# Optimization experiments

Hardware: AMD Instinct MI355X
Metric: run time of the kernel (lower is better)

## Reference

```python
import jax, jax.numpy as jnp
import numpy as np

B, S, D, H, F = 8, 1024, 1024, 16, 4096
DH = D // H
EPS = 1e-8
NEG_INF = -1e30


def setup_inputs() -> dict:
    key = jax.random.key(0)
    ks = jax.random.split(key, 12)
    x = jax.random.normal(ks[0], (B, S, D), jnp.float32)
    # variable valid lengths in [S//2, S]; True = keep (valid token)
    lengths = jax.random.randint(ks[1], (B,), S // 2, S + 1)
    src_key_padding_mask = jnp.arange(S)[None, :] < lengths[:, None]
    rel_pos_bias = 0.02 * jax.random.normal(ks[2], (1, H, S, S), jnp.float32)
    w = lambda k, sh, std: std * jax.random.normal(k, sh, jnp.float32)
    std = D ** -0.5
    return {
        'x': x,
        'src_key_padding_mask': src_key_padding_mask,
        'rel_pos_bias': rel_pos_bias,
        'Wq': w(ks[3], (D, D), std),
        'Wk': w(ks[4], (D, D), std),
        'Wv': w(ks[5], (D, D), std),
        'Wo': w(ks[6], (D, D), std),
        'g1': jnp.ones((D,), jnp.float32),
        'g2': jnp.ones((D,), jnp.float32),
        'W1': w(ks[7], (D, F), std),
        'b1': jnp.zeros((F,), jnp.float32),
        'W2': w(ks[8], (F, F and D), F ** -0.5),
        'b2': jnp.zeros((D,), jnp.float32),
    }


def rmsnorm(x, g):
    # x / sqrt(mean(x^2) + eps) * g   (no mean subtraction)
    ms = jnp.mean(x * x, axis=-1, keepdims=True)
    return x * jax.lax.rsqrt(ms + EPS) * g


def attention(h, kpm, rel_pos_bias, Wq, Wk, Wv, Wo):
    b, s, d = h.shape
    q = (h @ Wq).reshape(b, s, H, DH)
    k = (h @ Wk).reshape(b, s, H, DH)
    v = (h @ Wv).reshape(b, s, H, DH)
    scores = jnp.einsum('bqhd,bkhd->bhqk', q, k) / np.sqrt(DH)
    scores = scores + rel_pos_bias
    scores = jnp.where(kpm[:, None, None, :], scores, NEG_INF)
    attn = jax.nn.softmax(scores, axis=-1)
    out = jnp.einsum('bhqk,bkhd->bqhd', attn, v).reshape(b, s, d)
    return out @ Wo


def reference(x, src_key_padding_mask, rel_pos_bias,
              Wq, Wk, Wv, Wo, g1, g2, W1, b1, W2, b2):
    h = rmsnorm(x, g1)
    x = x + attention(h, src_key_padding_mask, rel_pos_bias, Wq, Wk, Wv, Wo)
    h = rmsnorm(x, g2)
    ff = jax.nn.relu(h @ W1 + b1) @ W2 + b2
    return x + ff
```

## Files before the change

### kernel.cpp

```cpp
#include <hip/hip_runtime.h>
#include <stdint.h>

typedef __bf16 bf16;
typedef __bf16 bf16x4 __attribute__((ext_vector_type(4)));
typedef __bf16 bf16x8 __attribute__((ext_vector_type(8)));
typedef float f32x4 __attribute__((ext_vector_type(4)));

constexpr int Bz = 8, S = 1024, D = 1024, NH = 16, DH = 64, F = 4096;

__device__ __forceinline__ bool is_f32(const uint16_t* dt) { return dt[0] == 0; }

__device__ __forceinline__ void ld4(const void* p, size_t idx, bool f32, float o[4]) {
  if (f32) {
    float4 v = *(const float4*)((const float*)p + idx);
    o[0] = v.x; o[1] = v.y; o[2] = v.z; o[3] = v.w;
  } else {
    bf16x4 v = *(const bf16x4*)((const bf16*)p + idx);
    o[0] = v[0]; o[1] = v[1]; o[2] = v[2]; o[3] = v[3];
  }
}

__device__ __forceinline__ float ld1(const void* p, size_t idx, bool f32) {
  return f32 ? ((const float*)p)[idx] : (float)((const bf16*)p)[idx];
}

__device__ __forceinline__ void gload_lds16(const bf16* g, bf16* l) {
  __builtin_amdgcn_global_load_lds(
      (const __attribute__((address_space(1))) void*)g,
      (__attribute__((address_space(3))) void*)l, 16, 0, 0);
}

__global__ void lengths_kernel(const unsigned char* __restrict__ mask,
                               int* __restrict__ lengths) {
  int b = blockIdx.x;
  int esz = (mask[1] == 1) ? 1 : ((mask[1] != 0) ? 2 : 4);
  int cnt = 0;
  for (int s = threadIdx.x; s < S; s += blockDim.x) {
    const unsigned char* p = mask + ((size_t)b * S + s) * esz;
    unsigned v = 0;
    for (int j = 0; j < esz; j++) v |= p[j];
    cnt += (v != 0) ? 1 : 0;
  }
#pragma unroll
  for (int m = 32; m >= 1; m >>= 1) cnt += __shfl_xor(cnt, m);
  __shared__ int sred[4];
  if ((threadIdx.x & 63) == 0) sred[threadIdx.x >> 6] = cnt;
  __syncthreads();
  if (threadIdx.x == 0) lengths[b] = sred[0] + sred[1] + sred[2] + sred[3];
}

__global__ void prep_all(const void* __restrict__ sq, const void* __restrict__ sk,
                         const void* __restrict__ sv, const void* __restrict__ so,
                         const void* __restrict__ s1, const void* __restrict__ s2,
                         bf16* __restrict__ dq, bf16* __restrict__ dk,
                         bf16* __restrict__ dv, bf16* __restrict__ do_,
                         bf16* __restrict__ d1, bf16* __restrict__ d2,
                         const void* __restrict__ rpb, bf16* __restrict__ biasb,
                         const uint16_t* __restrict__ dt) {
  bool f32 = is_f32(dt);
  int t = blockIdx.x;
  int tx = threadIdx.x, ty = threadIdx.y;
  if (t >= 3072) {
    size_t i = ((size_t)(t - 3072) * 256 + ty * 16 + tx) * 4;
    float v[4];
    ld4(rpb, i, f32, v);
    bf16x4 o;
#pragma unroll
    for (int j = 0; j < 4; j++) o[j] = (bf16)(v[j] * 1.4426950408889634f);
    *(bf16x4*)(biasb + i) = o;
    return;
  }
  const void* src;
  bf16* dst;
  int R, C, gx, base;
  if (t < 1024) {
    int wsel = t >> 8;
    base = wsel << 8;
    src = wsel == 0 ? sq : wsel == 1 ? sk : wsel == 2 ? sv : so;
    dst = wsel == 0 ? dq : wsel == 1 ? dk : wsel == 2 ? dv : do_;
    R = 1024; C = 1024; gx = 16;
  } else if (t < 2048) {
    base = 1024; src = s1; dst = d1; R = 1024; C = 4096; gx = 64;
  } else {
    base = 2048; src = s2; dst = d2; R = 4096; C = 1024; gx = 16;
  }
  int rel = t - base;
  int c0 = (rel % gx) * 64, r0 = (rel / gx) * 64;
  __shared__ bf16 tile[64][65];
#pragma unroll
  for (int i = 0; i < 4; i++) {
    int r = ty * 4 + i;
    float v[4];
    ld4(src, (size_t)(r0 + r) * C + c0 + tx * 4, f32, v);
#pragma unroll
    for (int j = 0; j < 4; j++) tile[r][tx * 4 + j] = (bf16)v[j];
  }
  __syncthreads();
#pragma unroll
  for (int i = 0; i < 4; i++) {
    int rr = ty * 4 + i;
    bf16x4 ov;
#pragma unroll
    for (int j = 0; j < 4; j++) ov[j] = tile[tx * 4 + j][rr];
    *(bf16x4*)(dst + (size_t)(c0 + rr) * R + r0 + tx * 4) = ov;
  }
}

template <bool ADD>
__global__ void rmsnorm_kernel(const void* __restrict__ xv, const bf16* __restrict__ add,
                               const void* __restrict__ gv, bf16* __restrict__ y,
                               const uint16_t* __restrict__ dt) {
  bool f32 = is_f32(dt);
  int row = blockIdx.x, t = threadIdx.x;
  float xf[4];
  ld4(xv, (size_t)row * D + t * 4, f32, xf);
  if (ADD) {
    bf16x4 a = *(const bf16x4*)(add + (size_t)row * D + t * 4);
#pragma unroll
    for (int j = 0; j < 4; j++) xf[j] += (float)a[j];
  }
  float ss = xf[0] * xf[0] + xf[1] * xf[1] + xf[2] * xf[2] + xf[3] * xf[3];
#pragma unroll
  for (int m = 32; m >= 1; m >>= 1) ss += __shfl_xor(ss, m);
  __shared__ float sred[4];
  if ((t & 63) == 0) sred[t >> 6] = ss;
  __syncthreads();
  float tot = sred[0] + sred[1] + sred[2] + sred[3];
  float scale = rsqrtf(tot * (1.0f / D) + 1e-8f);
  float gf[4];
  ld4(gv, (size_t)t * 4, f32, gf);
  bf16x4 ov;
#pragma unroll
  for (int j = 0; j < 4; j++) ov[j] = (bf16)(xf[j] * scale * gf[j]);
  *(bf16x4*)(y + (size_t)row * D + t * 4) = ov;
}

template <bool BIAS, bool RELU, bool RES1, bool RES2, bool OUTEXT, bool VT>
__global__ void gemm_nt(const bf16* __restrict__ A, const bf16* __restrict__ Bt,
                        void* __restrict__ Cv, const void* __restrict__ biasv,
                        const void* __restrict__ res1, const bf16* __restrict__ res2,
                        int M, int N, int K, const uint16_t* __restrict__ dt) {
  bool f32 = is_f32(dt);
  __shared__ bf16 As[2 * 4096];
  __shared__ bf16 Bs[2 * 4096];
  const int tid = threadIdx.x, lane = tid & 63, w = tid >> 6;
  const int wm = w >> 1, wn = w & 1;
  const int lid = blockIdx.x;
  const int bm = ((lid & 7) << 3) + ((lid >> 3) & 7);
  const int bn = lid >> 6;
  const int quad = lane >> 4, c = lane & 15;

  f32x4 acc[4][4];
#pragma unroll
  for (int i = 0; i < 4; i++)
#pragma unroll
    for (int j = 0; j < 4; j++)
#pragma unroll
      for (int r = 0; r < 4; r++) acc[i][j][r] = 0.f;

  const bf16* gA = A + (size_t)(bm * 128 + w * 16 + (lane >> 2)) * K + (lane & 3) * 8;
  const bf16* gB = Bt + (size_t)(bn * 128 + w * 16 + (lane >> 2)) * K + (lane & 3) * 8;
  bf16* lA = As + w * 512;
  bf16* lB = Bs + w * 512;
  const size_t rstep = (size_t)64 * K;

  int aoff[4], boff[4];
#pragma unroll
  for (int i = 0; i < 4; i++) {
    aoff[i] = (wm * 64 + i * 16 + c) * 32 + quad * 8;
    boff[i] = (wn * 64 + i * 16 + c) * 32 + quad * 8;
  }

  for (int k0 = 0; k0 < K; k0 += 64) {
    __syncthreads();
#pragma unroll
    for (int p = 0; p < 2; p++) {
      gload_lds16(gA + p * 32, lA + p * 4096);
      gload_lds16(gA + p * 32 + rstep, lA + p * 4096 + 2048);
      gload_lds16(gB + p * 32, lB + p * 4096);
      gload_lds16(gB + p * 32 + rstep, lB + p * 4096 + 2048);
    }
    gA += 64;
    gB += 64;
    __syncthreads();
#pragma unroll
    for (int p = 0; p < 2; p++) {
      bf16x8 af[4], bfr[4];
#pragma unroll
      for (int i = 0; i < 4; i++) af[i] = *(const bf16x8*)(As + p * 4096 + aoff[i]);
#pragma unroll
      for (int i = 0; i < 4; i++) bfr[i] = *(const bf16x8*)(Bs + p * 4096 + boff[i]);
#pragma unroll
      for (int i = 0; i < 4; i++)
#pragma unroll
        for (int j = 0; j < 4; j++)
          acc[i][j] = __builtin_amdgcn_mfma_f32_16x16x32_bf16(af[i], bfr[j], acc[i][j], 0, 0, 0);
    }
  }

  const int m0 = bm * 128 + wm * 64, n0 = bn * 128 + wn * 64;
#pragma unroll
  for (int i = 0; i < 4; i++) {
#pragma unroll
    for (int j = 0; j < 4; j++) {
      int col = n0 + j * 16 + c;
      if (VT) {
        int row0 = m0 + i * 16 + quad * 4;
        int bb = row0 >> 10, s0 = row0 & 1023;
        int hh = col >> 6, dd = col & 63;
        bf16x4 ov;
#pragma unroll
        for (int r = 0; r < 4; r++) ov[r] = (bf16)acc[i][j][r];
        *(bf16x4*)((bf16*)Cv + ((size_t)((bb << 4) + hh) * 64 + dd) * 1024 + s0) = ov;
      } else {
        float bv = BIAS ? ld1(biasv, col, f32) : 0.f;
#pragma unroll
        for (int r = 0; r < 4; r++) {
          int row = m0 + i * 16 + quad * 4 + r;
          size_t idx = (size_t)row * N + col;
          float vv = acc[i][j][r] + bv;
          if (RELU) vv = fmaxf(vv, 0.f);
          if (RES1) vv += ld1(res1, idx, f32);
          if (RES2) vv += (float)res2[idx];
          if (OUTEXT && f32) ((float*)Cv)[idx] = vv;
          else ((bf16*)Cv)[idx] = (bf16)vv;
        }
      }
    }
  }
}

#define SYNC()                            \
  do {                                    \
    __builtin_amdgcn_sched_barrier(0);    \
    __builtin_amdgcn_s_barrier();         \
    __builtin_amdgcn_sched_barrier(0);    \
  } while (0)
#define VMW(n)                                              \
  do {                                                      \
    asm volatile("s_waitcnt vmcnt(" #n ")" ::: "memory");   \
    __builtin_amdgcn_sched_barrier(0);                      \
  } while (0)

#define STA_(nb, rowbase, kb)                                                  \
  do {                                                                         \
    gload_lds16(Ag + (size_t)(rowbase) * K + (kb), &Abuf[nb][(rowbase) * 64]); \
    gload_lds16(Ag + (size_t)((rowbase) + 8) * K + (kb),                       \
                &Abuf[nb][((rowbase) + 8) * 64]);                              \
  } while (0)
#define STB_(nb, rowbase, kb)                                                  \
  do {                                                                         \
    gload_lds16(Bg + (size_t)(rowbase) * K + (kb), &Bbuf[nb][(rowbase) * 64]); \
    gload_lds16(Bg + (size_t)((rowbase) + 8) * K + (kb),                       \
                &Bbuf[nb][((rowbase) + 8) * 64]);                              \
  } while (0)
#define RDA_(MQ, fr, bufsel)                                                          \
  do {                                                                                \
    _Pragma("unroll") for (int ii = 0; ii < 4; ii++) {                                \
      int arow = wm * 128 + ((MQ)*4 + ii) * 16 + c;                                   \
      fr[ii][0] = *(const bf16x8*)&Abuf[bufsel][arow * 64 + ((quad ^ sx) * 8)];       \
      fr[ii][1] = *(const bf16x8*)&Abuf[bufsel][arow * 64 + (((4 + quad) ^ sx) * 8)]; \
    }                                                                                 \
  } while (0)
#define RDB_(NQ, fr, bufsel)                                                          \
  do {                                                                                \
    _Pragma("unroll") for (int jj = 0; jj < 2; jj++) {                                \
      int brow = wn * 64 + ((NQ)*2 + jj) * 16 + c;                                    \
      fr[jj][0] = *(const bf16x8*)&Bbuf[bufsel][brow * 64 + ((quad ^ sx) * 8)];       \
      fr[jj][1] = *(const bf16x8*)&Bbuf[bufsel][brow * 64 + (((4 + quad) ^ sx) * 8)]; \
    }                                                                                 \
  } while (0)

template <int MQ, int NQ>
__device__ __forceinline__ void mm_phase(f32x4 (&acc)[8][4], const bf16x8 (&afr)[4][2],
                                         const bf16x8 (&bfr)[2][2]) {
#pragma unroll
  for (int ii = 0; ii < 4; ii++)
#pragma unroll
    for (int jj = 0; jj < 2; jj++) {
      acc[MQ * 4 + ii][NQ * 2 + jj] = __builtin_amdgcn_mfma_f32_16x16x32_bf16(
          afr[ii][0], bfr[jj][0], acc[MQ * 4 + ii][NQ * 2 + jj], 0, 0, 0);
      acc[MQ * 4 + ii][NQ * 2 + jj] = __builtin_amdgcn_mfma_f32_16x16x32_bf16(
          afr[ii][1], bfr[jj][1], acc[MQ * 4 + ii][NQ * 2 + jj], 0, 0, 0);
    }
}

template <bool BIAS, bool RELU, bool QKV>
__global__ void __launch_bounds__(512, 2) gemm256(
    const bf16* __restrict__ A, const bf16* __restrict__ Bt, bf16* __restrict__ C,
    bf16* __restrict__ C2, const void* __restrict__ biasv, int N, int K,
    const uint16_t* __restrict__ dt) {
  bool f32 = is_f32(dt);
  __shared__ bf16 Abuf[2][256 * 64];
  __shared__ bf16 Bbuf[2][256 * 64];
  const int tid = threadIdx.x, lane = tid & 63, w = tid >> 6;
  const int wm = w >> 2, wn = w & 3;
  const int quad = lane >> 4, c = lane & 15;
  const int sx = c & 7;
  const int nbn = N >> 8;
  const int nwg = gridDim.x;
  const int sid = (blockIdx.x & 7) * (nwg >> 3) + (blockIdx.x >> 3);
  const int bm = sid / nbn, bn = sid % nbn;

  const int lrow = lane >> 3;
  const int lslot = ((lane & 7) ^ lrow) * 8;
  const bf16* Ag = A + (size_t)(bm * 256 + lrow) * K + lslot;
  const bf16* Bg = Bt + (size_t)(bn * 256 + lrow) * K + lslot;

  const int ra0 = wm * 128 + wn * 16;
  const int ra1 = ra0 + 64;
  const int rb0 = (wn >> 1) * 128 + (wn & 1) * 64 + wm * 16;
  const int rb1 = rb0 + 32;

  f32x4 acc[8][4];
#pragma unroll
  for (int i = 0; i < 8; i++)
#pragma unroll
    for (int j = 0; j < 4; j++)
#pragma unroll
      for (int r = 0; r < 4; r++) acc[i][j][r] = 0.f;

  const int nt = K >> 6;

  STA_(0, ra0, 0);
  STA_(0, ra1, 0);
  STB_(0, rb0, 0);
  STB_(0, rb1, 0);
  STA_(1, ra0, 64);
  VMW(2);
  SYNC();

  for (int t = 0; t < nt; ++t) {
    const int buf = t & 1, nb = buf ^ 1;
    const int kb1 = (t + 1) << 6, kb2 = (t + 2) << 6;
    const bool st1 = (t + 1 < nt), st2 = (t + 2 < nt);
    bf16x8 afr[4][2], bfr0[2][2], bfr1[2][2];
    RDA_(0, afr, buf);
    RDB_(0, bfr0, buf);
    if (st1) STA_(nb, ra1, kb1);
    SYNC();
    __builtin_amdgcn_s_setprio(1);
    mm_phase<0, 0>(acc, afr, bfr0);
    __builtin_amdgcn_s_setprio(0);
    VMW(2);
    SYNC();
    RDB_(1, bfr1, buf);
    if (st1) STB_(nb, rb0, kb1);
    SYNC();
    __builtin_amdgcn_s_setprio(1);
    mm_phase<0, 1>(acc, afr, bfr1);
    __builtin_amdgcn_s_setprio(0);
    SYNC();
    RDA_(1, afr, buf);
    if (st2) STA_(buf, ra0, kb2);
    SYNC();
    __builtin_amdgcn_s_setprio(1);
    mm_phase<1, 0>(acc, afr, bfr0);
    __builtin_amdgcn_s_setprio(0);
    SYNC();
    if (st1) STB_(nb, rb1, kb1);
    SYNC();
    __builtin_amdgcn_s_setprio(1);
    mm_phase<1, 1>(acc, afr, bfr1);
    __builtin_amdgcn_s_setprio(0);
    VMW(4);
    SYNC();
  }

  const int m0 = bm * 256 + wm * 128, n0 = bn * 256 + wn * 64;
  if (QKV && n0 >= 2048) {
#pragma unroll
    for (int fi = 0; fi < 8; fi++)
#pragma unroll
      for (int fj = 0; fj < 4; fj++) {
        int vcol = n0 + fj * 16 + c - 2048;
        int hh = vcol >> 6, dd = vcol & 63;
        int row0 = m0 + fi * 16 + quad * 4;
        int bb = row0 >> 10, s0 = row0 & 1023;
        bf16x4 ov;
#pragma unroll
        for (int r = 0; r < 4; r++) ov[r] = (bf16)acc[fi][fj][r];
        *(bf16x4*)(C2 + ((size_t)((bb << 4) + hh) * 64 + dd) * 1024 + s0) = ov;
      }
    return;
  }
  const int ldc = QKV ? 2048 : N;
#pragma unroll
  for (int fi = 0; fi < 8; fi++)
#pragma unroll
    for (int fj = 0; fj < 4; fj++) {
      int col = n0 + fj * 16 + c;
      float bv = BIAS ? ld1(biasv, col, f32) : 0.f;
#pragma unroll
      for (int r = 0; r < 4; r++) {
        int row = m0 + fi * 16 + quad * 4 + r;
        float vv = acc[fi][fj][r] + bv;
        if (RELU) vv = fmaxf(vv, 0.f);
        C[(size_t)row * ldc + col] = (bf16)vv;
      }
    }
}

__global__ void __launch_bounds__(256) attn_kernel(
    const bf16* __restrict__ qk, const bf16* __restrict__ vt,
    const bf16* __restrict__ bias, const int* __restrict__ lengths,
    bf16* __restrict__ out) {
  __shared__ bf16 QPs[64 * 72];
  __shared__ bf16 Ks[64][72];
  __shared__ bf16 Vs[64][72];
  const int tid = threadIdx.x, lane = tid & 63, w = tid >> 6;
  const int id = blockIdx.x;
  const int qt = id >> 7, b = (id >> 4) & 7, h = id & 15;
  const int len = lengths[b];
  const int quad = lane >> 4, c = lane & 15;
  const int r4 = tid >> 2, c4 = tid & 3;

  {
    size_t qrow = (size_t)(b * S + qt * 64 + r4) * 2048 + h * 64 + c4 * 8;
    *(bf16x8*)&QPs[r4 * 72 + c4 * 8] = *(const bf16x8*)&qk[qrow];
    *(bf16x8*)&QPs[r4 * 72 + 32 + c4 * 8] = *(const bf16x8*)&qk[qrow + 32];
  }
  __syncthreads();
  const bf16x8 a0 = *(const bf16x8*)&QPs[(w * 16 + c) * 72 + quad * 8];
  const bf16x8 a1 = *(const bf16x8*)&QPs[(w * 16 + c) * 72 + 32 + quad * 8];

  bf16* Pw = QPs + w * 16 * 72;
  const int xsw = (quad & 2) << 3;
  const int xsr = (c & 8) << 1;

  float l_[4] = {0.f, 0.f, 0.f, 0.f};
  f32x4 o[4];
#pragma unroll
  for (int ni = 0; ni < 4; ni++)
#pragma unroll
    for (int r = 0; r < 4; r++) o[ni][r] = 0.f;

  const bf16* bbp = bias + (size_t)h * S * S + (size_t)(qt * 64 + w * 16 + quad * 4) * S;
  const int nkt = (len + 63) >> 6;

  const size_t KSTEP = (size_t)64 * 2048;
  const bf16* gk = qk + (size_t)(b * S + r4) * 2048 + 1024 + h * 64 + c4 * 8;
  const bf16* gv = vt + ((size_t)((b * 16 + h) * 64 + r4)) * 1024 + c4 * 8;
  bf16x8 kr0 = *(const bf16x8*)gk;
  bf16x8 kr1 = *(const bf16x8*)(gk + 32);
  bf16x8 vr0 = *(const bf16x8*)gv;
  bf16x8 vr1 = *(const bf16x8*)(gv + 32);
  gk += KSTEP;
  gv += 64;

  for (int kt = 0; kt < nkt; kt++) {
    __syncthreads();
    *(bf16x8*)&Ks[r4][c4 * 8] = kr0;
    *(bf16x8*)&Ks[r4][32 + c4 * 8] = kr1;
    *(bf16x8*)&Vs[r4][c4 * 8] = vr0;
    *(bf16x8*)&Vs[r4][32 + c4 * 8] = vr1;
    __syncthreads();

    bf16 br[4][4];
#pragma unroll
    for (int ni = 0; ni < 4; ni++)
#pragma unroll
      for (int r = 0; r < 4; r++) br[ni][r] = bbp[(size_t)r * S + ni * 16 + c];

    if (kt + 1 < nkt) {
      kr0 = *(const bf16x8*)gk;
      kr1 = *(const bf16x8*)(gk + 32);
      vr0 = *(const bf16x8*)gv;
      vr1 = *(const bf16x8*)(gv + 32);
      gk += KSTEP;
      gv += 64;
    }

    f32x4 s[4];
#pragma unroll
    for (int ni = 0; ni < 4; ni++)
#pragma unroll
      for (int r = 0; r < 4; r++) s[ni][r] = 0.f;
#pragma unroll
    for (int ni = 0; ni < 4; ni++) {
      bf16x8 b0 = *(const bf16x8*)&Ks[ni * 16 + c][quad * 8];
      bf16x8 b1 = *(const bf16x8*)&Ks[ni * 16 + c][32 + quad * 8];
      s[ni] = __builtin_amdgcn_mfma_f32_16x16x32_bf16(a0, b0, s[ni], 0, 0, 0);
      s[ni] = __builtin_amdgcn_mfma_f32_16x16x32_bf16(a1, b1, s[ni], 0, 0, 0);
    }

    const bool full = (kt * 64 + 64 <= len);
#pragma unroll
    for (int ni = 0; ni < 4; ni++) {
      int col = kt * 64 + ni * 16 + c;
      bool valid = full || (col < len);
#pragma unroll
      for (int r = 0; r < 4; r++) {
        float p = valid ? exp2f(fmaf(s[ni][r], 0.18033688011112042f, (float)br[ni][r])) : 0.f;
        s[ni][r] = p;
        l_[r] += p;
      }
    }

#pragma unroll
    for (int ni = 0; ni < 4; ni++)
#pragma unroll
      for (int r = 0; r < 4; r++)
        Pw[(quad * 4 + r) * 72 + ((ni * 16 + c) ^ xsw)] = (bf16)s[ni][r];

    bf16x8 p0 = *(const bf16x8*)&Pw[c * 72 + ((quad * 8) ^ xsr)];
    bf16x8 p1 = *(const bf16x8*)&Pw[c * 72 + ((32 + quad * 8) ^ xsr)];
#pragma unroll
    for (int ni = 0; ni < 4; ni++) {
      bf16x8 vb0 = *(const bf16x8*)&Vs[ni * 16 + c][quad * 8];
      bf16x8 vb1 = *(const bf16x8*)&Vs[ni * 16 + c][32 + quad * 8];
      o[ni] = __builtin_amdgcn_mfma_f32_16x16x32_bf16(p0, vb0, o[ni], 0, 0, 0);
      o[ni] = __builtin_amdgcn_mfma_f32_16x16x32_bf16(p1, vb1, o[ni], 0, 0, 0);
    }
    bbp += 64;
  }

  float inv[4];
#pragma unroll
  for (int r = 0; r < 4; r++) {
    float l = l_[r];
    l += __shfl_xor(l, 1);
    l += __shfl_xor(l, 2);
    l += __shfl_xor(l, 4);
    l += __shfl_xor(l, 8);
    inv[r] = 1.f / l;
  }
#pragma unroll
  for (int ni = 0; ni < 4; ni++)
#pragma unroll
    for (int r = 0; r < 4; r++) {
      size_t idx = ((size_t)(b * S + qt * 64 + w * 16 + quad * 4 + r)) * D + h * 64 + ni * 16 + c;
      out[idx] = (bf16)(o[ni][r] * inv[r]);
    }
}

extern "C" void kernel_launch(void* const* d_in, const int* in_sizes, int n_in,
                              void* d_out, int out_size, void* d_ws, size_t ws_size,
                              hipStream_t stream) {
  const void* x = d_in[0];
  const unsigned char* mask = (const unsigned char*)d_in[1];
  const void* rpb = d_in[2];
  const void* Wq = d_in[3];
  const void* Wk = d_in[4];
  const void* Wv = d_in[5];
  const void* Wo = d_in[6];
  const void* g1 = d_in[7];
  const void* g2 = d_in[8];
  const void* W1 = d_in[9];
  const void* b1 = d_in[10];
  const void* W2 = d_in[11];
  const void* b2 = d_in[12];
  const uint16_t* dt = (const uint16_t*)d_in[7];

  char* ws = (char*)d_ws;
  const size_t MB = 1024 * 1024;
  bf16* WqkT = (bf16*)(ws + 0 * MB);
  bf16* WkT = (bf16*)(ws + 2 * MB);
  bf16* WvT = (bf16*)(ws + 4 * MB);
  bf16* WoT = (bf16*)(ws + 6 * MB);
  bf16* W1T = (bf16*)(ws + 8 * MB);
  bf16* W2T = (bf16*)(ws + 16 * MB);
  bf16* hbuf = (bf16*)(ws + 24 * MB);
  bf16* qkbuf = (bf16*)(ws + 40 * MB);
  bf16* d1buf = (bf16*)(ws + 40 * MB);
  bf16* vtbuf = (bf16*)(ws + 72 * MB);
  bf16* biasb = (bf16*)(ws + 88 * MB);
  bf16* a1b = (bf16*)(ws + 56 * MB);
  int* lens = (int*)d_out;

  lengths_kernel<<<dim3(8), dim3(256), 0, stream>>>(mask, lens);
  prep_all<<<dim3(3072 + 16384), dim3(16, 16), 0, stream>>>(
      Wq, Wk, Wv, Wo, W1, W2, WqkT, WkT, WvT, WoT, W1T, W2T, rpb, biasb, dt);

  rmsnorm_kernel<false><<<dim3(8192), dim3(256), 0, stream>>>(x, nullptr, g1, hbuf, dt);
  gemm256<false, false, true><<<dim3(384), dim3(512), 0, stream>>>(
      hbuf, WqkT, qkbuf, vtbuf, nullptr, 3072, 1024, dt);
  attn_kernel<<<dim3(2048), dim3(256), 0, stream>>>(qkbuf, vtbuf, biasb, lens, hbuf);
  gemm_nt<false, false, false, false, false, false><<<dim3(8 * 64), dim3(256), 0, stream>>>(
      hbuf, WoT, d1buf, nullptr, nullptr, nullptr, 8192, 1024, 1024, dt);
  rmsnorm_kernel<true><<<dim3(8192), dim3(256), 0, stream>>>(x, d1buf, g2, hbuf, dt);
  gemm256<true, true, false><<<dim3(512), dim3(512), 0, stream>>>(
      hbuf, W1T, a1b, nullptr, b1, 4096, 1024, dt);
  gemm_nt<true, false, true, true, true, false><<<dim3(8 * 64), dim3(256), 0, stream>>>(
      a1b, W2T, d_out, b2, x, d1buf, 8192, 1024, 4096, dt);

  (void)in_sizes; (void)n_in; (void)out_size; (void)ws_size;
}
```

Before: 536.9 us.

## Read fp32 relative-position bias directly in attention and fold lengths into prep

Removes the separate pass that converted the relative position bias to scaled bf16, and has the attention kernel read the original bias tensor and scale by log2(e) inline. The bias for the next key tile is register-prefetched during the PV MFMAs. The mask-length computation becomes extra blocks of the weight-prep kernel, dropping one launch. This saves a 64MB read plus 32MB write of bias, but attention now reads fp32 bias (twice the bytes per block, scalar loads) and uses more registers.

```diff
diff --git a/kernel.cpp b/kernel.cpp
--- a/kernel.cpp
+++ b/kernel.cpp
@@ -30,44 +30,36 @@
       (__attribute__((address_space(3))) void*)l, 16, 0, 0);
 }
 
-__global__ void lengths_kernel(const unsigned char* __restrict__ mask,
-                               int* __restrict__ lengths) {
-  int b = blockIdx.x;
-  int esz = (mask[1] == 1) ? 1 : ((mask[1] != 0) ? 2 : 4);
-  int cnt = 0;
-  for (int s = threadIdx.x; s < S; s += blockDim.x) {
-    const unsigned char* p = mask + ((size_t)b * S + s) * esz;
-    unsigned v = 0;
-    for (int j = 0; j < esz; j++) v |= p[j];
-    cnt += (v != 0) ? 1 : 0;
-  }
-#pragma unroll
-  for (int m = 32; m >= 1; m >>= 1) cnt += __shfl_xor(cnt, m);
-  __shared__ int sred[4];
-  if ((threadIdx.x & 63) == 0) sred[threadIdx.x >> 6] = cnt;
-  __syncthreads();
-  if (threadIdx.x == 0) lengths[b] = sred[0] + sred[1] + sred[2] + sred[3];
-}
-
 __global__ void prep_all(const void* __restrict__ sq, const void* __restrict__ sk,
                          const void* __restrict__ sv, const void* __restrict__ so,
                          const void* __restrict__ s1, const void* __restrict__ s2,
                          bf16* __restrict__ dq, bf16* __restrict__ dk,
                          bf16* __restrict__ dv, bf16* __restrict__ do_,
                          bf16* __restrict__ d1, bf16* __restrict__ d2,
-                         const void* __restrict__ rpb, bf16* __restrict__ biasb,
+                         const unsigned char* __restrict__ mask,
+                         int* __restrict__ lengths,
                          const uint16_t* __restrict__ dt) {
+  __shared__ bf16 tile[64][65];
+  __shared__ int sred[4];
   bool f32 = is_f32(dt);
   int t = blockIdx.x;
   int tx = threadIdx.x, ty = threadIdx.y;
   if (t >= 3072) {
-    size_t i = ((size_t)(t - 3072) * 256 + ty * 16 + tx) * 4;
-    float v[4];
-    ld4(rpb, i, f32, v);
-    bf16x4 o;
-#pragma unroll
-    for (int j = 0; j < 4; j++) o[j] = (bf16)(v[j] * 1.4426950408889634f);
-    *(bf16x4*)(biasb + i) = o;
+    int b = t - 3072;
+    int tid = ty * 16 + tx;
+    int esz = (mask[1] == 1) ? 1 : ((mask[1] != 0) ? 2 : 4);
+    int cnt = 0;
+    for (int s = tid; s < S; s += 256) {
+      const unsigned char* p = mask + ((size_t)b * S + s) * esz;
+      unsigned v = 0;
+      for (int j = 0; j < esz; j++) v |= p[j];
+      cnt += (v != 0) ? 1 : 0;
+    }
+#pragma unroll
+    for (int m = 32; m >= 1; m >>= 1) cnt += __shfl_xor(cnt, m);
+    if ((tid & 63) == 0) sred[tid >> 6] = cnt;
+    __syncthreads();
+    if (tid == 0) lengths[b] = sred[0] + sred[1] + sred[2] + sred[3];
     return;
   }
   const void* src;
@@ -86,7 +78,6 @@
   }
   int rel = t - base;
   int c0 = (rel % gx) * 64, r0 = (rel / gx) * 64;
-  __shared__ bf16 tile[64][65];
 #pragma unroll
   for (int i = 0; i < 4; i++) {
     int r = ty * 4 + i;
@@ -403,11 +394,12 @@
 
 __global__ void __launch_bounds__(256) attn_kernel(
     const bf16* __restrict__ qk, const bf16* __restrict__ vt,
-    const bf16* __restrict__ bias, const int* __restrict__ lengths,
-    bf16* __restrict__ out) {
+    const void* __restrict__ bias, const int* __restrict__ lengths,
+    bf16* __restrict__ out, const uint16_t* __restrict__ dt) {
   __shared__ bf16 QPs[64 * 72];
   __shared__ bf16 Ks[64][72];
   __shared__ bf16 Vs[64][72];
+  const bool f32 = is_f32(dt);
   const int tid = threadIdx.x, lane = tid & 63, w = tid >> 6;
   const int id = blockIdx.x;
   const int qt = id >> 7, b = (id >> 4) & 7, h = id & 15;
@@ -435,8 +427,9 @@
 #pragma unroll
     for (int r = 0; r < 4; r++) o[ni][r] = 0.f;
 
-  const bf16* bbp = bias + (size_t)h * S * S + (size_t)(qt * 64 + w * 16 + quad * 4) * S;
+  const size_t bb0 = (size_t)h * S * S + (size_t)(qt * 64 + w * 16 + quad * 4) * S + c;
   const int nkt = (len + 63) >> 6;
+  const float LOG2E = 1.4426950408889634f;
 
   const size_t KSTEP = (size_t)64 * 2048;
   const bf16* gk = qk + (size_t)(b * S + r4) * 2048 + 1024 + h * 64 + c4 * 8;
@@ -447,6 +440,12 @@
   bf16x8 vr1 = *(const bf16x8*)(gv + 32);
   gk += KSTEP;
   gv += 64;
+  float brf[4][4];
+#pragma unroll
+  for (int ni = 0; ni < 4; ni++)
+#pragma unroll
+    for (int r = 0; r < 4; r++)
+      brf[ni][r] = ld1(bias, bb0 + (size_t)r * S + ni * 16, f32) * LOG2E;
 
   for (int kt = 0; kt < nkt; kt++) {
     __syncthreads();
@@ -456,12 +455,6 @@
     *(bf16x8*)&Vs[r4][32 + c4 * 8] = vr1;
     __syncthreads();
 
-    bf16 br[4][4];
-#pragma unroll
-    for (int ni = 0; ni < 4; ni++)
-#pragma unroll
-      for (int r = 0; r < 4; r++) br[ni][r] = bbp[(size_t)r * S + ni * 16 + c];
-
     if (kt + 1 < nkt) {
       kr0 = *(const bf16x8*)gk;
       kr1 = *(const bf16x8*)(gk + 32);
@@ -491,7 +484,7 @@
       bool valid = full || (col < len);
 #pragma unroll
       for (int r = 0; r < 4; r++) {
-        float p = valid ? exp2f(fmaf(s[ni][r], 0.18033688011112042f, (float)br[ni][r])) : 0.f;
+        float p = valid ? exp2f(fmaf(s[ni][r], 0.18033688011112042f, brf[ni][r])) : 0.f;
         s[ni][r] = p;
         l_[r] += p;
       }
@@ -505,6 +498,17 @@
 
     bf16x8 p0 = *(const bf16x8*)&Pw[c * 72 + ((quad * 8) ^ xsr)];
     bf16x8 p1 = *(const bf16x8*)&Pw[c * 72 + ((32 + quad * 8) ^ xsr)];
+
+    float brn[4][4];
+    if (kt + 1 < nkt) {
+      const size_t bnext = bb0 + (size_t)(kt + 1) * 64;
+#pragma unroll
+      for (int ni = 0; ni < 4; ni++)
+#pragma unroll
+        for (int r = 0; r < 4; r++)
+          brn[ni][r] = ld1(bias, bnext + (size_t)r * S + ni * 16, f32) * LOG2E;
+    }
+
 #pragma unroll
     for (int ni = 0; ni < 4; ni++) {
       bf16x8 vb0 = *(const bf16x8*)&Vs[ni * 16 + c][quad * 8];
@@ -512,7 +516,12 @@
       o[ni] = __builtin_amdgcn_mfma_f32_16x16x32_bf16(p0, vb0, o[ni], 0, 0, 0);
       o[ni] = __builtin_amdgcn_mfma_f32_16x16x32_bf16(p1, vb1, o[ni], 0, 0, 0);
     }
-    bbp += 64;
+    if (kt + 1 < nkt) {
+#pragma unroll
+      for (int ni = 0; ni < 4; ni++)
+#pragma unroll
+        for (int r = 0; r < 4; r++) brf[ni][r] = brn[ni][r];
+    }
   }
 
   float inv[4];
@@ -564,18 +573,16 @@
   bf16* qkbuf = (bf16*)(ws + 40 * MB);
   bf16* d1buf = (bf16*)(ws + 40 * MB);
   bf16* vtbuf = (bf16*)(ws + 72 * MB);
-  bf16* biasb = (bf16*)(ws + 88 * MB);
   bf16* a1b = (bf16*)(ws + 56 * MB);
   int* lens = (int*)d_out;
 
-  lengths_kernel<<<dim3(8), dim3(256), 0, stream>>>(mask, lens);
-  prep_all<<<dim3(3072 + 16384), dim3(16, 16), 0, stream>>>(
-      Wq, Wk, Wv, Wo, W1, W2, WqkT, WkT, WvT, WoT, W1T, W2T, rpb, biasb, dt);
+  prep_all<<<dim3(3080), dim3(16, 16), 0, stream>>>(
+      Wq, Wk, Wv, Wo, W1, W2, WqkT, WkT, WvT, WoT, W1T, W2T, mask, lens, dt);
 
   rmsnorm_kernel<false><<<dim3(8192), dim3(256), 0, stream>>>(x, nullptr, g1, hbuf, dt);
   gemm256<false, false, true><<<dim3(384), dim3(512), 0, stream>>>(
       hbuf, WqkT, qkbuf, vtbuf, nullptr, 3072, 1024, dt);
-  attn_kernel<<<dim3(2048), dim3(256), 0, stream>>>(qkbuf, vtbuf, biasb, lens, hbuf);
+  attn_kernel<<<dim3(2048), dim3(256), 0, stream>>>(qkbuf, vtbuf, rpb, lens, hbuf, dt);
   gemm_nt<false, false, false, false, false, false><<<dim3(8 * 64), dim3(256), 0, stream>>>(
       hbuf, WoT, d1buf, nullptr, nullptr, nullptr, 8192, 1024, 1024, dt);
   rmsnorm_kernel<true><<<dim3(8192), dim3(256), 0, stream>>>(x, d1buf, g2, hbuf, dt);
```

Measured after the change: 541.8 us. No clear change (+0.9%).

## Double-buffer K/V tiles in attention, add MFMA priority, fold lengths into prep

Applied to the files above, without the earlier changes.

The attention kernel now keeps two LDS buffers for K and V, so the next tile is written to LDS while the current one is being used. This replaces two barriers per iteration with one. The MFMA sections are wrapped in s_setprio to favour matrix-issuing waves. The separate lengths kernel is merged into prep_all as eight extra blocks, which removes one launch. The cost is more LDS per block, which may reduce occupancy.

```diff
diff --git a/kernel.cpp b/kernel.cpp
--- a/kernel.cpp
+++ b/kernel.cpp
@@ -30,44 +30,47 @@
       (__attribute__((address_space(3))) void*)l, 16, 0, 0);
 }
 
-__global__ void lengths_kernel(const unsigned char* __restrict__ mask,
-                               int* __restrict__ lengths) {
-  int b = blockIdx.x;
-  int esz = (mask[1] == 1) ? 1 : ((mask[1] != 0) ? 2 : 4);
-  int cnt = 0;
-  for (int s = threadIdx.x; s < S; s += blockDim.x) {
-    const unsigned char* p = mask + ((size_t)b * S + s) * esz;
-    unsigned v = 0;
-    for (int j = 0; j < esz; j++) v |= p[j];
-    cnt += (v != 0) ? 1 : 0;
-  }
-#pragma unroll
-  for (int m = 32; m >= 1; m >>= 1) cnt += __shfl_xor(cnt, m);
-  __shared__ int sred[4];
-  if ((threadIdx.x & 63) == 0) sred[threadIdx.x >> 6] = cnt;
-  __syncthreads();
-  if (threadIdx.x == 0) lengths[b] = sred[0] + sred[1] + sred[2] + sred[3];
-}
-
 __global__ void prep_all(const void* __restrict__ sq, const void* __restrict__ sk,
                          const void* __restrict__ sv, const void* __restrict__ so,
                          const void* __restrict__ s1, const void* __restrict__ s2,
                          bf16* __restrict__ dq, bf16* __restrict__ dk,
                          bf16* __restrict__ dv, bf16* __restrict__ do_,
                          bf16* __restrict__ d1, bf16* __restrict__ d2,
+                         const unsigned char* __restrict__ mask,
+                         int* __restrict__ lengths,
                          const void* __restrict__ rpb, bf16* __restrict__ biasb,
                          const uint16_t* __restrict__ dt) {
+  __shared__ bf16 tile[64][65];
+  __shared__ int sred[4];
   bool f32 = is_f32(dt);
   int t = blockIdx.x;
   int tx = threadIdx.x, ty = threadIdx.y;
-  if (t >= 3072) {
-    size_t i = ((size_t)(t - 3072) * 256 + ty * 16 + tx) * 4;
+  if (t >= 3080) {
+    size_t i = ((size_t)(t - 3080) * 256 + ty * 16 + tx) * 4;
     float v[4];
     ld4(rpb, i, f32, v);
     bf16x4 o;
 #pragma unroll
     for (int j = 0; j < 4; j++) o[j] = (bf16)(v[j] * 1.4426950408889634f);
     *(bf16x4*)(biasb + i) = o;
+    return;
+  }
+  if (t >= 3072) {
+    int b = t - 3072;
+    int tid = ty * 16 + tx;
+    int esz = (mask[1] == 1) ? 1 : ((mask[1] != 0) ? 2 : 4);
+    int cnt = 0;
+    for (int s = tid; s < S; s += 256) {
+      const unsigned char* p = mask + ((size_t)b * S + s) * esz;
+      unsigned v = 0;
+      for (int j = 0; j < esz; j++) v |= p[j];
+      cnt += (v != 0) ? 1 : 0;
+    }
+#pragma unroll
+    for (int m = 32; m >= 1; m >>= 1) cnt += __shfl_xor(cnt, m);
+    if ((tid & 63) == 0) sred[tid >> 6] = cnt;
+    __syncthreads();
+    if (tid == 0) lengths[b] = sred[0] + sred[1] + sred[2] + sred[3];
     return;
   }
   const void* src;
@@ -86,7 +89,6 @@
   }
   int rel = t - base;
   int c0 = (rel % gx) * 64, r0 = (rel / gx) * 64;
-  __shared__ bf16 tile[64][65];
 #pragma unroll
   for (int i = 0; i < 4; i++) {
     int r = ty * 4 + i;
@@ -406,8 +408,8 @@
     const bf16* __restrict__ bias, const int* __restrict__ lengths,
     bf16* __restrict__ out) {
   __shared__ bf16 QPs[64 * 72];
-  __shared__ bf16 Ks[64][72];
-  __shared__ bf16 Vs[64][72];
+  __shared__ bf16 Ks[2][64][72];
+  __shared__ bf16 Vs[2][64][72];
   const int tid = threadIdx.x, lane = tid & 63, w = tid >> 6;
   const int id = blockIdx.x;
   const int qt = id >> 7, b = (id >> 4) & 7, h = id & 15;
@@ -447,14 +449,36 @@
   bf16x8 vr1 = *(const bf16x8*)(gv + 32);
   gk += KSTEP;
   gv += 64;
+  *(bf16x8*)&Ks[0][r4][c4 * 8] = kr0;
+  *(bf16x8*)&Ks[0][r4][32 + c4 * 8] = kr1;
+  *(bf16x8*)&Vs[0][r4][c4 * 8] = vr0;
+  *(bf16x8*)&Vs[0][r4][32 + c4 * 8] = vr1;
+  if (nkt > 1) {
+    kr0 = *(const bf16x8*)gk;
+    kr1 = *(const bf16x8*)(gk + 32);
+    vr0 = *(const bf16x8*)gv;
+    vr1 = *(const bf16x8*)(gv + 32);
+    gk += KSTEP;
+    gv += 64;
+  }
+  __syncthreads();
 
   for (int kt = 0; kt < nkt; kt++) {
-    __syncthreads();
-    *(bf16x8*)&Ks[r4][c4 * 8] = kr0;
-    *(bf16x8*)&Ks[r4][32 + c4 * 8] = kr1;
-    *(bf16x8*)&Vs[r4][c4 * 8] = vr0;
-    *(bf16x8*)&Vs[r4][32 + c4 * 8] = vr1;
-    __syncthreads();
+    const int buf = kt & 1, nb = buf ^ 1;
+    if (kt + 1 < nkt) {
+      *(bf16x8*)&Ks[nb][r4][c4 * 8] = kr0;
+      *(bf16x8*)&Ks[nb][r4][32 + c4 * 8] = kr1;
+      *(bf16x8*)&Vs[nb][r4][c4 * 8] = vr0;
+      *(bf16x8*)&Vs[nb][r4][32 + c4 * 8] = vr1;
+      if (kt + 2 < nkt) {
+        kr0 = *(const bf16x8*)gk;
+        kr1 = *(const bf16x8*)(gk + 32);
+        vr0 = *(const bf16x8*)gv;
+        vr1 = *(const bf16x8*)(gv + 32);
+        gk += KSTEP;
+        gv += 64;
+      }
+    }
 
     bf16 br[4][4];
 #pragma unroll
@@ -462,27 +486,20 @@
 #pragma unroll
       for (int r = 0; r < 4; r++) br[ni][r] = bbp[(size_t)r * S + ni * 16 + c];
 
-    if (kt + 1 < nkt) {
-      kr0 = *(const bf16x8*)gk;
-      kr1 = *(const bf16x8*)(gk + 32);
-      vr0 = *(const bf16x8*)gv;
-      vr1 = *(const bf16x8*)(gv + 32);
-      gk += KSTEP;
-      gv += 64;
-    }
-
     f32x4 s[4];
 #pragma unroll
     for (int ni = 0; ni < 4; ni++)
 #pragma unroll
       for (int r = 0; r < 4; r++) s[ni][r] = 0.f;
+    __builtin_amdgcn_s_setprio(1);
 #pragma unroll
     for (int ni = 0; ni < 4; ni++) {
-      bf16x8 b0 = *(const bf16x8*)&Ks[ni * 16 + c][quad * 8];
-      bf16x8 b1 = *(const bf16x8*)&Ks[ni * 16 + c][32 + quad * 8];
+      bf16x8 b0 = *(const bf16x8*)&Ks[buf][ni * 16 + c][quad * 8];
+      bf16x8 b1 = *(const bf16x8*)&Ks[buf][ni * 16 + c][32 + quad * 8];
       s[ni] = __builtin_amdgcn_mfma_f32_16x16x32_bf16(a0, b0, s[ni], 0, 0, 0);
       s[ni] = __builtin_amdgcn_mfma_f32_16x16x32_bf16(a1, b1, s[ni], 0, 0, 0);
     }
+    __builtin_amdgcn_s_setprio(0);
 
     const bool full = (kt * 64 + 64 <= len);
 #pragma unroll
@@ -505,14 +522,17 @@
 
     bf16x8 p0 = *(const bf16x8*)&Pw[c * 72 + ((quad * 8) ^ xsr)];
     bf16x8 p1 = *(const bf16x8*)&Pw[c * 72 + ((32 + quad * 8) ^ xsr)];
+    __builtin_amdgcn_s_setprio(1);
 #pragma unroll
     for (int ni = 0; ni < 4; ni++) {
-      bf16x8 vb0 = *(const bf16x8*)&Vs[ni * 16 + c][quad * 8];
-      bf16x8 vb1 = *(const bf16x8*)&Vs[ni * 16 + c][32 + quad * 8];
+      bf16x8 vb0 = *(const bf16x8*)&Vs[buf][ni * 16 + c][quad * 8];
+      bf16x8 vb1 = *(const bf16x8*)&Vs[buf][ni * 16 + c][32 + quad * 8];
       o[ni] = __builtin_amdgcn_mfma_f32_16x16x32_bf16(p0, vb0, o[ni], 0, 0, 0);
       o[ni] = __builtin_amdgcn_mfma_f32_16x16x32_bf16(p1, vb1, o[ni], 0, 0, 0);
     }
+    __builtin_amdgcn_s_setprio(0);
     bbp += 64;
+    __syncthreads();
   }
 
   float inv[4];
@@ -568,9 +588,8 @@
   bf16* a1b = (bf16*)(ws + 56 * MB);
   int* lens = (int*)d_out;
 
-  lengths_kernel<<<dim3(8), dim3(256), 0, stream>>>(mask, lens);
-  prep_all<<<dim3(3072 + 16384), dim3(16, 16), 0, stream>>>(
-      Wq, Wk, Wv, Wo, W1, W2, WqkT, WkT, WvT, WoT, W1T, W2T, rpb, biasb, dt);
+  prep_all<<<dim3(3080 + 16384), dim3(16, 16), 0, stream>>>(
+      Wq, Wk, Wv, Wo, W1, W2, WqkT, WkT, WvT, WoT, W1T, W2T, mask, lens, rpb, biasb, dt);
 
   rmsnorm_kernel<false><<<dim3(8192), dim3(256), 0, stream>>>(x, nullptr, g1, hbuf, dt);
   gemm256<false, false, true><<<dim3(384), dim3(512), 0, stream>>>(
```

New measurement: 534.3 us. About the same (-0.5%).
